# Kernel optimization log

Hardware: AMD Instinct MI355X
Metric: run time of the kernel (lower is better)

Reference implementation:

```python
import jax, jax.numpy as jnp
import numpy as np

K = 4  # Chebyshev order (init arg)


def setup_inputs() -> dict:
    key = jax.random.key(0)
    k1, k2, k3, k4, k5 = jax.random.split(key, 5)
    N, M, Fin, Fout, E = 4, 100000, 32, 64, 1600000
    x = jax.random.normal(k1, (N, M, Fin), dtype=jnp.float32)
    edge_vals = jax.random.normal(k2, (E,), dtype=jnp.float32) * 0.1
    W = jax.random.normal(k3, (Fin * K, Fout), dtype=jnp.float32) * 0.05
    edge_rows = jax.random.randint(k4, (E,), 0, M, dtype=jnp.int32)
    edge_cols = jax.random.randint(k5, (E,), 0, M, dtype=jnp.int32)
    return {"x": x, "edge_vals": edge_vals, "W": W,
            "edge_rows": edge_rows, "edge_cols": edge_cols}


def reference(x, edge_vals, W, edge_rows, edge_cols):
    # x: [N, M, Fin]; L given in COO form (rows, cols, vals), shape [M, M].
    N, M, Fin = x.shape

    # [M, Fin*N] column-major-per-vertex layout, as in the original
    xt = jnp.transpose(x, (1, 2, 0)).reshape(M, Fin * N)

    def Lhat_matmul(v):
        # rescaled Laplacian: L' = 2*L/lmax - I with lmax=2  =>  L' v = L v - v
        gathered = edge_vals[:, None] * v[edge_cols]          # [E, Fin*N]
        Lv = jax.ops.segment_sum(gathered, edge_rows, num_segments=M)
        return Lv - v

    # Chebyshev recursion: T0 = x, T1 = L'x, T_k = 2 L' T_{k-1} - T_{k-2}
    Ts = [xt, Lhat_matmul(xt)]
    for _ in range(K - 2):
        Ts.append(2.0 * Lhat_matmul(Ts[-1]) - Ts[-2])
    xs = jnp.stack(Ts)                                        # [K, M, Fin*N]

    xs = xs.reshape(K, M, Fin, N).transpose(3, 1, 2, 0)       # [N, M, Fin, K]
    xs = xs.reshape(N * M, Fin * K)
    out = xs @ W                                              # [N*M, Fout]
    return out.reshape(N, M, W.shape[1])
```

## Files before the change

kernel.cpp:

```cpp
#include <hip/hip_runtime.h>
#include <hip/hip_bf16.h>
#include <stdint.h>

#define N_DIM 4
#define FIN 32
#define FOUT 64
#define ROWLEN 128
#define NBLK 256
#define BMAX 512

typedef __attribute__((ext_vector_type(4))) float f32x4;
typedef __attribute__((ext_vector_type(8))) short bf16x8;

__device__ __forceinline__ ushort f32_to_bf16_rn(float f) {
  uint u = __float_as_uint(f);
  u += 0x7FFFu + ((u >> 16) & 1u);
  return (ushort)(u >> 16);
}
__device__ __forceinline__ float bf16_lo(uint p) { return __uint_as_float(p << 16); }
__device__ __forceinline__ float bf16_hi(uint p) { return __uint_as_float(p & 0xFFFF0000u); }

__global__ void transpose_kernel(const float* __restrict__ x,
                                 ushort* __restrict__ Tb0, int M) {
  int i = blockIdx.x * blockDim.x + threadIdx.x;
  if (i >= M * 16) return;
  int m = i >> 4;
  int n = (i >> 2) & 3;
  int f8 = i & 3;
  const float* src = x + ((size_t)n * M + m) * FIN + f8 * 8;
  float4 v0 = *reinterpret_cast<const float4*>(src);
  float4 v1 = *reinterpret_cast<const float4*>(src + 4);
  ushort h[8];
  h[0] = f32_to_bf16_rn(v0.x); h[1] = f32_to_bf16_rn(v0.y);
  h[2] = f32_to_bf16_rn(v0.z); h[3] = f32_to_bf16_rn(v0.w);
  h[4] = f32_to_bf16_rn(v1.x); h[5] = f32_to_bf16_rn(v1.y);
  h[6] = f32_to_bf16_rn(v1.z); h[7] = f32_to_bf16_rn(v1.w);
  *reinterpret_cast<uint4*>(Tb0 + (size_t)m * ROWLEN + n * 32 + f8 * 8) =
      *reinterpret_cast<const uint4*>(h);
}

__global__ __launch_bounds__(256) void bcount_kernel(
    const int* __restrict__ rows, int* __restrict__ c, int E, int B, int ce) {
  __shared__ int hist[BMAX];
  int tid = threadIdx.x, blk = blockIdx.x;
  for (int b = tid; b < B; b += 256) hist[b] = 0;
  __syncthreads();
  int start = blk * ce;
  int end = min(E, start + ce);
  for (int e = start + tid; e < end; e += 256)
    atomicAdd(&hist[rows[e] >> 8], 1);
  __syncthreads();
  for (int b = tid; b < B; b += 256) c[b * NBLK + blk] = hist[b];
}

__global__ __launch_bounds__(256) void bscanA_kernel(
    int* __restrict__ c, int* __restrict__ btot) {
  __shared__ int wsum[4];
  int b = blockIdx.x, tid = threadIdx.x;
  int lane = tid & 63, wid = tid >> 6;
  int v = c[b * NBLK + tid];
  int s = v;
#pragma unroll
  for (int off = 1; off < 64; off <<= 1) {
    int u = __shfl_up(s, off);
    if (lane >= off) s += u;
  }
  if (lane == 63) wsum[wid] = s;
  __syncthreads();
  if (tid == 0) {
    int run = 0;
#pragma unroll
    for (int w = 0; w < 4; ++w) { int t = wsum[w]; wsum[w] = run; run += t; }
  }
  __syncthreads();
  int excl = wsum[wid] + s - v;
  c[b * NBLK + tid] = excl;
  if (tid == 255) btot[b] = excl + v;
}

__global__ __launch_bounds__(512) void bscanB_kernel(
    const int* __restrict__ btot, int* __restrict__ bucket_start,
    int* __restrict__ row_start, int B, int M, int E) {
  __shared__ int wsum[8];
  int tid = threadIdx.x, lane = tid & 63, wid = tid >> 6;
  int v = (tid < B) ? btot[tid] : 0;
  int s = v;
#pragma unroll
  for (int off = 1; off < 64; off <<= 1) {
    int u = __shfl_up(s, off);
    if (lane >= off) s += u;
  }
  if (lane == 63) wsum[wid] = s;
  __syncthreads();
  if (tid == 0) {
    int run = 0;
#pragma unroll
    for (int w = 0; w < 8; ++w) { int t = wsum[w]; wsum[w] = run; run += t; }
  }
  __syncthreads();
  int excl = wsum[wid] + s - v;
  if (tid < B) bucket_start[tid] = excl;
  if (tid == 0) { bucket_start[B] = E; row_start[M] = E; }
}

__global__ __launch_bounds__(256) void bscatter_kernel(
    const int* __restrict__ rows, const int* __restrict__ cols,
    const float* __restrict__ vals, const int* __restrict__ c,
    const int* __restrict__ bucket_start, int2* __restrict__ binned,
    int E, int B, int ce) {
  __shared__ int base[BMAX];
  __shared__ int lcur[BMAX];
  int tid = threadIdx.x, blk = blockIdx.x;
  for (int b = tid; b < B; b += 256) {
    base[b] = bucket_start[b] + c[b * NBLK + blk];
    lcur[b] = 0;
  }
  __syncthreads();
  int start = blk * ce;
  int end = min(E, start + ce);
  for (int e = start + tid; e < end; e += 256) {
    int r = rows[e];
    int b = r >> 8;
    int pos = atomicAdd(&lcur[b], 1);
    binned[base[b] + pos] =
        make_int2(cols[e] | ((r & 255) << 17), __float_as_int(vals[e]));
  }
}

__global__ __launch_bounds__(256) void bsort_kernel(
    const int2* __restrict__ binned, const int* __restrict__ bucket_start,
    int2* __restrict__ csr, int* __restrict__ row_start, int M) {
  __shared__ int hist[256];
  __shared__ int wsum[4];
  int b = blockIdx.x, tid = threadIdx.x;
  int base = bucket_start[b];
  int cnt = bucket_start[b + 1] - base;
  hist[tid] = 0;
  __syncthreads();
  for (int i = tid; i < cnt; i += 256)
    atomicAdd(&hist[((unsigned)binned[base + i].x) >> 17], 1);
  __syncthreads();
  int v = hist[tid];
  int lane = tid & 63, wid = tid >> 6;
  int s = v;
#pragma unroll
  for (int off = 1; off < 64; off <<= 1) {
    int u = __shfl_up(s, off);
    if (lane >= off) s += u;
  }
  if (lane == 63) wsum[wid] = s;
  __syncthreads();
  if (tid == 0) {
    int run = 0;
#pragma unroll
    for (int w = 0; w < 4; ++w) { int t = wsum[w]; wsum[w] = run; run += t; }
  }
  __syncthreads();
  int excl = wsum[wid] + s - v;
  int r = (b << 8) + tid;
  if (r < M) row_start[r] = base + excl;
  __syncthreads();
  hist[tid] = excl;
  __syncthreads();
  for (int i = tid; i < cnt; i += 256) {
    int2 en = binned[base + i];
    int rl = ((unsigned)en.x) >> 17;
    int p = atomicAdd(&hist[rl], 1);
    csr[base + p] = make_int2(en.x & 0x1FFFF, en.y);
  }
}

#define LOADC(C, base)                                        \
  _Pragma("unroll") for (int u = 0; u < 8; ++u) C[u] = csr[(base) + u];
#define GATH(G, C)                                            \
  _Pragma("unroll") for (int u = 0; u < 8; ++u)               \
      G[u] = srcb[(size_t)(unsigned)C[u].x * 64 + lane];
#define CONS(G, C)                                            \
  _Pragma("unroll") for (int u = 0; u < 8; ++u) {             \
    float v = __int_as_float(C[u].y);                         \
    ax += v * bf16_lo(G[u]);                                  \
    ay += v * bf16_hi(G[u]);                                  \
  }

__global__ __launch_bounds__(256) void spmm_kernel(
    const uint* __restrict__ srcb, const uint* __restrict__ prevb,
    uint* __restrict__ dstb,
    const int* __restrict__ row_start, const int2* __restrict__ csr,
    int M, float alpha, float beta, float gamma) {
  int wid = __builtin_amdgcn_readfirstlane((int)threadIdx.x >> 6);
  int gw = blockIdx.x * 4 + wid;
  int lane = threadIdx.x & 63;
  if (gw >= M) return;
  int s = row_start[gw];
  int e = row_start[gw + 1];
  uint sp = srcb[(size_t)gw * 64 + lane];
  uint pp = prevb ? prevb[(size_t)gw * 64 + lane] : 0u;

  float ax = 0.f, ay = 0.f;
  int j = s;
  int cnt = e - s;
  if (cnt >= 16) {
    int2 c0[8], c1[8];
    uint g0[8], g1[8];
    LOADC(c0, j); GATH(g0, c0);
    LOADC(c1, j + 8); GATH(g1, c1);
    j += 16;
    for (; j + 16 <= e; j += 16) {
      CONS(g0, c0); LOADC(c0, j); GATH(g0, c0);
      CONS(g1, c1); LOADC(c1, j + 8); GATH(g1, c1);
    }
    if (j + 8 <= e) {
      CONS(g0, c0); LOADC(c0, j); GATH(g0, c0);
      j += 8;
      CONS(g1, c1);
      CONS(g0, c0);
    } else {
      CONS(g0, c0);
      CONS(g1, c1);
    }
  } else if (cnt >= 8) {
    int2 c0[8];
    uint g0[8];
    LOADC(c0, j); GATH(g0, c0);
    j += 8;
    CONS(g0, c0);
  }
  for (; j < e; ++j) {
    int2 cv = csr[j];
    uint p = srcb[(size_t)(unsigned)cv.x * 64 + lane];
    float v = __int_as_float(cv.y);
    ax += v * bf16_lo(p);
    ay += v * bf16_hi(p);
  }

  ax = alpha * ax + beta * bf16_lo(sp);
  ay = alpha * ay + beta * bf16_hi(sp);
  if (prevb) {
    ax += gamma * bf16_lo(pp);
    ay += gamma * bf16_hi(pp);
  }
  dstb[(size_t)gw * 64 + lane] =
      (uint)f32_to_bf16_rn(ax) | ((uint)f32_to_bf16_rn(ay) << 16);
}

__global__ __launch_bounds__(256) void gemm_kernel(
    const ushort* __restrict__ Tb0, const ushort* __restrict__ Tb1,
    const ushort* __restrict__ Tb2, const ushort* __restrict__ Tb3,
    const float* __restrict__ W, float* __restrict__ out,
    int M, int nwaves) {
  int lane = threadIdx.x & 63;
  int gwave = blockIdx.x * 4 + ((int)threadIdx.x >> 6);
  int g = lane >> 4;
  int q = lane & 15;

  bf16x8 b[4][4];
#pragma unroll
  for (int t = 0; t < 4; ++t) {
#pragma unroll
    for (int ft = 0; ft < 4; ++ft) {
#pragma unroll
      for (int e = 0; e < 8; ++e) {
        float w = W[((8 * g + e) * 4 + t) * FOUT + ft * 16 + q];
        b[t][ft][e] = (short)f32_to_bf16_rn(w);
      }
    }
  }

  int NT = (M + 3) >> 2;
  for (int tile = gwave; tile < NT; tile += nwaves) {
    int m0 = tile * 4;
    int mA = m0 + (q >> 2);
    if (mA > M - 1) mA = M - 1;
    int n = q & 3;
    size_t abase = (size_t)mA * ROWLEN + n * 32 + g * 8;

    f32x4 C0 = {0.f, 0.f, 0.f, 0.f};
    f32x4 C1 = C0, C2 = C0, C3 = C0;
#pragma unroll
    for (int t = 0; t < 4; ++t) {
      const ushort* Tb = t == 0 ? Tb0 : t == 1 ? Tb1 : t == 2 ? Tb2 : Tb3;
      bf16x8 a = *reinterpret_cast<const bf16x8*>(Tb + abase);
      C0 = __builtin_amdgcn_mfma_f32_16x16x32_bf16(a, b[t][0], C0, 0, 0, 0);
      C1 = __builtin_amdgcn_mfma_f32_16x16x32_bf16(a, b[t][1], C1, 0, 0, 0);
      C2 = __builtin_amdgcn_mfma_f32_16x16x32_bf16(a, b[t][2], C2, 0, 0, 0);
      C3 = __builtin_amdgcn_mfma_f32_16x16x32_bf16(a, b[t][3], C3, 0, 0, 0);
    }
    int mS = m0 + g;
    if (mS < M) {
#pragma unroll
      for (int r = 0; r < 4; ++r) {
        size_t ob = ((size_t)r * M + mS) * FOUT + q;
        out[ob +  0] = C0[r];
        out[ob + 16] = C1[r];
        out[ob + 32] = C2[r];
        out[ob + 48] = C3[r];
      }
    }
  }
}

extern "C" void kernel_launch(void* const* d_in, const int* in_sizes, int n_in,
                              void* d_out, int out_size, void* d_ws, size_t ws_size,
                              hipStream_t stream) {
  const float* x         = (const float*)d_in[0];
  const float* edge_vals = (const float*)d_in[1];
  const float* W         = (const float*)d_in[2];
  const int* edge_rows   = (const int*)d_in[3];
  const int* edge_cols   = (const int*)d_in[4];
  float* out = (float*)d_out;

  int M = in_sizes[0] / (N_DIM * FIN);
  int E = in_sizes[1];
  int B = (M + 255) >> 8;
  int ce = (E + NBLK - 1) / NBLK;

  char* ws = (char*)d_ws;
  size_t rowf = (size_t)M * ROWLEN;
  ushort* Tb0 = (ushort*)ws;
  ushort* Tb1 = Tb0 + rowf;
  ushort* Tb2 = Tb1 + rowf;
  ushort* Tb3 = Tb2 + rowf;
  int2* binned = (int2*)(Tb3 + rowf);
  int2* csr = binned + E;
  int* c = (int*)(csr + E);
  int* btot = c + (size_t)B * NBLK;
  int* bucket_start = btot + B;
  int* row_start = bucket_start + (B + 1);

  transpose_kernel<<<(M * 16 + 255) / 256, 256, 0, stream>>>(x, Tb0, M);
  bcount_kernel<<<NBLK, 256, 0, stream>>>(edge_rows, c, E, B, ce);
  bscanA_kernel<<<B, 256, 0, stream>>>(c, btot);
  bscanB_kernel<<<1, 512, 0, stream>>>(btot, bucket_start, row_start, B, M, E);
  bscatter_kernel<<<NBLK, 256, 0, stream>>>(edge_rows, edge_cols, edge_vals,
                                            c, bucket_start, binned, E, B, ce);
  bsort_kernel<<<B, 256, 0, stream>>>(binned, bucket_start, csr, row_start, M);

  int spmm_blocks = (M + 3) / 4;
  spmm_kernel<<<spmm_blocks, 256, 0, stream>>>(
      (const uint*)Tb0, nullptr, (uint*)Tb1, row_start, csr,
      M, 1.f, -1.f, 0.f);
  spmm_kernel<<<spmm_blocks, 256, 0, stream>>>(
      (const uint*)Tb1, (const uint*)Tb0, (uint*)Tb2, row_start, csr,
      M, 2.f, -2.f, -1.f);
  spmm_kernel<<<spmm_blocks, 256, 0, stream>>>(
      (const uint*)Tb2, (const uint*)Tb1, (uint*)Tb3, row_start, csr,
      M, 2.f, -2.f, -1.f);

  int gemm_blocks = 1024;
  gemm_kernel<<<gemm_blocks, 256, 0, stream>>>(
      Tb0, Tb1, Tb2, Tb3, W, out, M, gemm_blocks * 4);
}
```

Baseline: 309.5 us.

## Fuse preprocessing kernels and cache bucket entries in registers during sort

Merges the transpose and row-bucket histogram into one launch, and folds the second-level bucket scan into the scatter and sort kernels so each block recomputes its prefix. This removes two kernel launches and their serialization gaps. It also doubles the number of binning blocks and caches up to 20 entries per thread in registers in the sort kernel, so the binned array is read once instead of twice. The costs are redundant prefix computation in every block and higher register pressure in the sort kernel.

After: 297.0 us, median of 2. 1.04x faster.

```diff
diff --git a/kernel.cpp b/kernel.cpp
--- a/kernel.cpp
+++ b/kernel.cpp
@@ -6,8 +6,9 @@
 #define FIN 32
 #define FOUT 64
 #define ROWLEN 128
-#define NBLK 256
+#define NBLK 512
 #define BMAX 512
+#define MAXE 20
 
 typedef __attribute__((ext_vector_type(4))) float f32x4;
 typedef __attribute__((ext_vector_type(8))) short bf16x8;
@@ -20,8 +21,23 @@
 __device__ __forceinline__ float bf16_lo(uint p) { return __uint_as_float(p << 16); }
 __device__ __forceinline__ float bf16_hi(uint p) { return __uint_as_float(p & 0xFFFF0000u); }
 
-__global__ void transpose_kernel(const float* __restrict__ x,
-                                 ushort* __restrict__ Tb0, int M) {
+__global__ __launch_bounds__(256) void trans_count_kernel(
+    const float* __restrict__ x, ushort* __restrict__ Tb0, int M, int tblocks,
+    const int* __restrict__ rows, int* __restrict__ c, int E, int B, int ce) {
+  __shared__ int hist[BMAX];
+  if (blockIdx.x >= (unsigned)tblocks) {
+    int blk = blockIdx.x - tblocks;
+    int tid = threadIdx.x;
+    for (int b = tid; b < B; b += 256) hist[b] = 0;
+    __syncthreads();
+    int start = blk * ce;
+    int end = min(E, start + ce);
+    for (int e = start + tid; e < end; e += 256)
+      atomicAdd(&hist[rows[e] >> 8], 1);
+    __syncthreads();
+    for (int b = tid; b < B; b += 256) c[blk * B + b] = hist[b];
+    return;
+  }
   int i = blockIdx.x * blockDim.x + threadIdx.x;
   if (i >= M * 16) return;
   int m = i >> 4;
@@ -39,26 +55,13 @@
       *reinterpret_cast<const uint4*>(h);
 }
 
-__global__ __launch_bounds__(256) void bcount_kernel(
-    const int* __restrict__ rows, int* __restrict__ c, int E, int B, int ce) {
-  __shared__ int hist[BMAX];
-  int tid = threadIdx.x, blk = blockIdx.x;
-  for (int b = tid; b < B; b += 256) hist[b] = 0;
-  __syncthreads();
-  int start = blk * ce;
-  int end = min(E, start + ce);
-  for (int e = start + tid; e < end; e += 256)
-    atomicAdd(&hist[rows[e] >> 8], 1);
-  __syncthreads();
-  for (int b = tid; b < B; b += 256) c[b * NBLK + blk] = hist[b];
-}
-
-__global__ __launch_bounds__(256) void bscanA_kernel(
-    int* __restrict__ c, int* __restrict__ btot) {
-  __shared__ int wsum[4];
+__global__ __launch_bounds__(NBLK) void bscanA_kernel(
+    const int* __restrict__ c, int* __restrict__ cs,
+    int* __restrict__ btot, int B) {
+  __shared__ int wsum[8];
   int b = blockIdx.x, tid = threadIdx.x;
   int lane = tid & 63, wid = tid >> 6;
-  int v = c[b * NBLK + tid];
+  int v = c[tid * B + b];
   int s = v;
 #pragma unroll
   for (int off = 1; off < 64; off <<= 1) {
@@ -70,21 +73,30 @@
   if (tid == 0) {
     int run = 0;
 #pragma unroll
-    for (int w = 0; w < 4; ++w) { int t = wsum[w]; wsum[w] = run; run += t; }
+    for (int w = 0; w < 8; ++w) { int t = wsum[w]; wsum[w] = run; run += t; }
   }
   __syncthreads();
   int excl = wsum[wid] + s - v;
-  c[b * NBLK + tid] = excl;
-  if (tid == 255) btot[b] = excl + v;
-}
-
-__global__ __launch_bounds__(512) void bscanB_kernel(
-    const int* __restrict__ btot, int* __restrict__ bucket_start,
-    int* __restrict__ row_start, int B, int M, int E) {
-  __shared__ int wsum[8];
-  int tid = threadIdx.x, lane = tid & 63, wid = tid >> 6;
-  int v = (tid < B) ? btot[tid] : 0;
-  int s = v;
+  cs[b * NBLK + tid] = excl;
+  if (tid == NBLK - 1) btot[b] = excl + v;
+}
+
+__global__ __launch_bounds__(256) void bscatter_kernel(
+    const int* __restrict__ rows, const int* __restrict__ cols,
+    const float* __restrict__ vals, const int* __restrict__ cs,
+    const int* __restrict__ btot, int2* __restrict__ binned,
+    int E, int B, int ce) {
+  __shared__ int bstart[BMAX];
+  __shared__ int base[BMAX];
+  __shared__ int lcur[BMAX];
+  __shared__ int wsum[4];
+  int tid = threadIdx.x, blk = blockIdx.x;
+  int lane = tid & 63, wid = tid >> 6;
+  int i0 = 2 * tid, i1 = 2 * tid + 1;
+  int v0 = (i0 < B) ? btot[i0] : 0;
+  int v1 = (i1 < B) ? btot[i1] : 0;
+  int ps = v0 + v1;
+  int s = ps;
 #pragma unroll
   for (int off = 1; off < 64; off <<= 1) {
     int u = __shfl_up(s, off);
@@ -95,24 +107,15 @@
   if (tid == 0) {
     int run = 0;
 #pragma unroll
-    for (int w = 0; w < 8; ++w) { int t = wsum[w]; wsum[w] = run; run += t; }
-  }
-  __syncthreads();
-  int excl = wsum[wid] + s - v;
-  if (tid < B) bucket_start[tid] = excl;
-  if (tid == 0) { bucket_start[B] = E; row_start[M] = E; }
-}
-
-__global__ __launch_bounds__(256) void bscatter_kernel(
-    const int* __restrict__ rows, const int* __restrict__ cols,
-    const float* __restrict__ vals, const int* __restrict__ c,
-    const int* __restrict__ bucket_start, int2* __restrict__ binned,
-    int E, int B, int ce) {
-  __shared__ int base[BMAX];
-  __shared__ int lcur[BMAX];
-  int tid = threadIdx.x, blk = blockIdx.x;
+    for (int w = 0; w < 4; ++w) { int t = wsum[w]; wsum[w] = run; run += t; }
+  }
+  __syncthreads();
+  int excl = wsum[wid] + s - ps;
+  bstart[i0] = excl;
+  bstart[i1] = excl + v0;
+  __syncthreads();
   for (int b = tid; b < B; b += 256) {
-    base[b] = bucket_start[b] + c[b * NBLK + blk];
+    base[b] = bstart[b] + cs[b * NBLK + blk];
     lcur[b] = 0;
   }
   __syncthreads();
@@ -128,20 +131,41 @@
 }
 
 __global__ __launch_bounds__(256) void bsort_kernel(
-    const int2* __restrict__ binned, const int* __restrict__ bucket_start,
-    int2* __restrict__ csr, int* __restrict__ row_start, int M) {
+    const int2* __restrict__ binned, const int* __restrict__ btot,
+    int2* __restrict__ csr, int* __restrict__ row_start,
+    int M, int B, int E) {
   __shared__ int hist[256];
   __shared__ int wsum[4];
+  __shared__ int sbase;
   int b = blockIdx.x, tid = threadIdx.x;
-  int base = bucket_start[b];
-  int cnt = bucket_start[b + 1] - base;
+  int lane = tid & 63, wid = tid >> 6;
   hist[tid] = 0;
-  __syncthreads();
-  for (int i = tid; i < cnt; i += 256)
+  if (b == 0 && tid == 0) row_start[M] = E;
+  int acc = 0;
+  for (int i = tid; i < B; i += 256)
+    if (i < b) acc += btot[i];
+#pragma unroll
+  for (int off = 1; off < 64; off <<= 1) acc += __shfl_xor(acc, off);
+  if (lane == 0) wsum[wid] = acc;
+  __syncthreads();
+  if (tid == 0) sbase = wsum[0] + wsum[1] + wsum[2] + wsum[3];
+  __syncthreads();
+  int base = sbase;
+  int cnt = btot[b];
+
+  int2 en[MAXE];
+#pragma unroll
+  for (int k = 0; k < MAXE; ++k) {
+    int i = tid + k * 256;
+    if (i < cnt) {
+      en[k] = binned[base + i];
+      atomicAdd(&hist[((unsigned)en[k].x) >> 17], 1);
+    }
+  }
+  for (int i = tid + MAXE * 256; i < cnt; i += 256)
     atomicAdd(&hist[((unsigned)binned[base + i].x) >> 17], 1);
   __syncthreads();
   int v = hist[tid];
-  int lane = tid & 63, wid = tid >> 6;
   int s = v;
 #pragma unroll
   for (int off = 1; off < 64; off <<= 1) {
@@ -162,11 +186,20 @@
   __syncthreads();
   hist[tid] = excl;
   __syncthreads();
-  for (int i = tid; i < cnt; i += 256) {
-    int2 en = binned[base + i];
-    int rl = ((unsigned)en.x) >> 17;
+#pragma unroll
+  for (int k = 0; k < MAXE; ++k) {
+    int i = tid + k * 256;
+    if (i < cnt) {
+      int rl = ((unsigned)en[k].x) >> 17;
+      int p = atomicAdd(&hist[rl], 1);
+      csr[base + p] = make_int2(en[k].x & 0x1FFFF, en[k].y);
+    }
+  }
+  for (int i = tid + MAXE * 256; i < cnt; i += 256) {
+    int2 e2 = binned[base + i];
+    int rl = ((unsigned)e2.x) >> 17;
     int p = atomicAdd(&hist[rl], 1);
-    csr[base + p] = make_int2(en.x & 0x1FFFF, en.y);
+    csr[base + p] = make_int2(e2.x & 0x1FFFF, e2.y);
   }
 }
 
@@ -313,6 +346,7 @@
   int E = in_sizes[1];
   int B = (M + 255) >> 8;
   int ce = (E + NBLK - 1) / NBLK;
+  int tblocks = (M * 16 + 255) / 256;
 
   char* ws = (char*)d_ws;
   size_t rowf = (size_t)M * ROWLEN;
@@ -322,18 +356,17 @@
   ushort* Tb3 = Tb2 + rowf;
   int2* binned = (int2*)(Tb3 + rowf);
   int2* csr = binned + E;
-  int* c = (int*)(csr + E);
-  int* btot = c + (size_t)B * NBLK;
-  int* bucket_start = btot + B;
-  int* row_start = bucket_start + (B + 1);
-
-  transpose_kernel<<<(M * 16 + 255) / 256, 256, 0, stream>>>(x, Tb0, M);
-  bcount_kernel<<<NBLK, 256, 0, stream>>>(edge_rows, c, E, B, ce);
-  bscanA_kernel<<<B, 256, 0, stream>>>(c, btot);
-  bscanB_kernel<<<1, 512, 0, stream>>>(btot, bucket_start, row_start, B, M, E);
+  int* c = (int*)(csr + E + 8);
+  int* cs = c + (size_t)NBLK * B;
+  int* btot = cs + (size_t)NBLK * B;
+  int* row_start = btot + B;
+
+  trans_count_kernel<<<tblocks + NBLK, 256, 0, stream>>>(
+      x, Tb0, M, tblocks, edge_rows, c, E, B, ce);
+  bscanA_kernel<<<B, NBLK, 0, stream>>>(c, cs, btot, B);
   bscatter_kernel<<<NBLK, 256, 0, stream>>>(edge_rows, edge_cols, edge_vals,
-                                            c, bucket_start, binned, E, B, ce);
-  bsort_kernel<<<B, 256, 0, stream>>>(binned, bucket_start, csr, row_start, M);
+                                            cs, btot, binned, E, B, ce);
+  bsort_kernel<<<B, 256, 0, stream>>>(binned, btot, csr, row_start, M, B, E);
 
   int spmm_blocks = (M + 3) / 4;
   spmm_kernel<<<spmm_blocks, 256, 0, stream>>>(
```
